# Optimization experiments

Hardware: AMD Instinct MI355X
Metric: run time of the kernel (lower is better)

## Reference

```python
import jax, jax.numpy as jnp
import numpy as np

N = 20000        # nodes
E = 160000       # directed edges (self-loops added in reference, as PyG GATConv does)
IN = 128         # in_channels
OUT = 128        # out_channels
H = 36           # heads of conv1 (head kwarg)
C = 36           # per-head channels of conv1 (== head kwarg)
HID = H * C      # 1296, conv1 concat output
NEG_SLOPE = 0.2  # PyG GATConv default


def gat_layer(x, src, dst, W, a_src, a_dst, bias, heads, ch, concat, num_nodes):
    """One PyG-style GATConv (eval mode, self-loops already in src/dst)."""
    h = (x @ W).reshape(num_nodes, heads, ch)               # [N,H,C]
    alpha_s = jnp.sum(h * a_src, axis=-1)                   # [N,H]
    alpha_d = jnp.sum(h * a_dst, axis=-1)                   # [N,H]
    e = jax.nn.leaky_relu(alpha_s[src] + alpha_d[dst], NEG_SLOPE)  # [E,H]
    # segment softmax over incoming edges of each target node
    m = jax.ops.segment_max(e, dst, num_segments=num_nodes)        # [N,H]
    m = jnp.where(jnp.isfinite(m), m, 0.0)                  # nodes with no in-edges
    ex = jnp.exp(e - m[dst])                                # [E,H]
    denom = jax.ops.segment_sum(ex, dst, num_segments=num_nodes)   # [N,H]
    alpha = ex / (denom[dst] + 1e-16)                       # [E,H]
    # weighted scatter-aggregate of source features
    out = jax.ops.segment_sum(h[src] * alpha[:, :, None], dst, num_segments=num_nodes)  # [N,H,C]
    out = out.reshape(num_nodes, heads * ch) if concat else out.mean(axis=1)
    return out + bias


def setup_inputs() -> dict:
    key = jax.random.key(0)
    ks = jax.random.split(key, 12)
    x = jax.random.normal(ks[0], (N, IN), jnp.float32)
    edge_index = jax.random.randint(ks[1], (2, E), 0, N, dtype=jnp.int64)
    # conv1 params: heads=36, out per head=36, concat
    W1 = jax.random.normal(ks[2], (IN, H * C), jnp.float32) / np.float32(np.sqrt(IN))
    a_src1 = jax.random.normal(ks[3], (H, C), jnp.float32) * 0.1
    a_dst1 = jax.random.normal(ks[4], (H, C), jnp.float32) * 0.1
    b1 = jnp.zeros((HID,), jnp.float32)
    # conv2 params: heads=1, out=OUT, no concat
    W2 = jax.random.normal(ks[5], (HID, OUT), jnp.float32) / np.float32(np.sqrt(HID))
    a_src2 = jax.random.normal(ks[6], (1, OUT), jnp.float32) * 0.1
    a_dst2 = jax.random.normal(ks[7], (1, OUT), jnp.float32) * 0.1
    b2 = jnp.zeros((OUT,), jnp.float32)
    return {"x": x, "edge_index": edge_index,
            "W1": W1, "a_src1": a_src1, "a_dst1": a_dst1, "b1": b1,
            "W2": W2, "a_src2": a_src2, "a_dst2": a_dst2, "b2": b2}


def reference(x, edge_index, W1, a_src1, a_dst1, b1, W2, a_src2, a_dst2, b2):
    num_nodes = x.shape[0]
    loop = jnp.arange(num_nodes, dtype=edge_index.dtype)
    src = jnp.concatenate([edge_index[0], loop])   # add self-loops (PyG default)
    dst = jnp.concatenate([edge_index[1], loop])
    h = jax.nn.relu(gat_layer(x, src, dst, W1, a_src1, a_dst1, b1,
                              heads=H, ch=C, concat=True, num_nodes=num_nodes))
    out = jax.nn.relu(gat_layer(h, src, dst, W2, a_src2, a_dst2, b2,
                                heads=1, ch=OUT, concat=False, num_nodes=num_nodes))
    return out
```

## Files before the change

kernel.cpp:

```cpp
#include <hip/hip_runtime.h>

#define N_NODES 20000
#define E_EDGES 160000
#define ET (E_EDGES + N_NODES)
#define IN_CH 128
#define HID 1296
#define HEADS 36
#define CPH 36
#define OUT_CH 128
#define KP2 1344
#define NEG_SLOPE 0.2f

typedef __attribute__((ext_vector_type(8))) short bf16x8;
typedef __attribute__((ext_vector_type(4))) float floatx4;

__device__ __forceinline__ float bf2f(unsigned short u) {
    union { unsigned int i; float f; } c; c.i = ((unsigned int)u) << 16; return c.f;
}
__device__ __forceinline__ unsigned short f2bf(float f) {
    union { float f; unsigned int i; } c; c.f = f;
    unsigned int r = c.i + 0x7FFF + ((c.i >> 16) & 1);
    return (unsigned short)(r >> 16);
}

#define NX (N_NODES * IN_CH / 4)
#define NW1 (HID * IN_CH)
#define NW2 (OUT_CH * KP2)
__global__ __launch_bounds__(256) void k_prep(const float* __restrict__ x,
                                              unsigned short* __restrict__ xb,
                                              const float* __restrict__ W1,
                                              unsigned short* __restrict__ W1T,
                                              const float* __restrict__ W2,
                                              unsigned short* __restrict__ W2T) {
    int gid = blockIdx.x * 256 + threadIdx.x;
    if (gid < NX) {
        float4 v = ((const float4*)x)[gid];
        ushort4 o; o.x = f2bf(v.x); o.y = f2bf(v.y); o.z = f2bf(v.z); o.w = f2bf(v.w);
        ((ushort4*)xb)[gid] = o;
    } else if (gid < NX + NW1) {
        int g = gid - NX;
        int n = g >> 7, k = g & 127;
        W1T[g] = f2bf(W1[(size_t)k * HID + n]);
    } else if (gid < NX + NW1 + NW2) {
        int g = gid - NX - NW1;
        int n = g / KP2, k = g - n * KP2;
        W2T[g] = (k < HID) ? f2bf(W2[(size_t)k * OUT_CH + n]) : 0;
    }
}

__global__ __launch_bounds__(256) void k_gemm1(const unsigned short* __restrict__ xb,
                                               const unsigned short* __restrict__ W1T,
                                               unsigned short* __restrict__ h1b) {
    __shared__ unsigned short As[128][136];
    __shared__ unsigned short Bs[64][136];
    int tid = threadIdx.x;
    int r0 = blockIdx.x * 128;
    int n0 = blockIdx.y * 64;
#pragma unroll
    for (int i = 0; i < 8; i++) {
        int c = tid + i * 256;
        int row = c >> 4, kc = (c & 15) * 8;
        int gr = min(r0 + row, N_NODES - 1);
        *(bf16x8*)&As[row][kc] = *(const bf16x8*)(xb + (size_t)gr * IN_CH + kc);
    }
#pragma unroll
    for (int i = 0; i < 4; i++) {
        int c = tid + i * 256;
        int row = c >> 4, kc = (c & 15) * 8;
        int gn = min(n0 + row, HID - 1);
        *(bf16x8*)&Bs[row][kc] = *(const bf16x8*)(W1T + (size_t)gn * IN_CH + kc);
    }
    __syncthreads();
    int lane = tid & 63, w = tid >> 6;
    int quad = lane >> 4, l15 = lane & 15;
    int mbase = w * 32;
    floatx4 acc[2][4];
#pragma unroll
    for (int i = 0; i < 2; i++)
#pragma unroll
        for (int j = 0; j < 4; j++) acc[i][j] = (floatx4){0.f, 0.f, 0.f, 0.f};
#pragma unroll
    for (int kc = 0; kc < 128; kc += 32) {
        bf16x8 a0 = *(const bf16x8*)&As[mbase + l15][kc + quad * 8];
        bf16x8 a1 = *(const bf16x8*)&As[mbase + 16 + l15][kc + quad * 8];
#pragma unroll
        for (int j = 0; j < 4; j++) {
            bf16x8 b = *(const bf16x8*)&Bs[j * 16 + l15][kc + quad * 8];
            acc[0][j] = __builtin_amdgcn_mfma_f32_16x16x32_bf16(a0, b, acc[0][j], 0, 0, 0);
            acc[1][j] = __builtin_amdgcn_mfma_f32_16x16x32_bf16(a1, b, acc[1][j], 0, 0, 0);
        }
    }
#pragma unroll
    for (int i = 0; i < 2; i++)
#pragma unroll
        for (int j = 0; j < 4; j++) {
            int colc = n0 + j * 16 + l15;
            if (colc >= HID) continue;
#pragma unroll
            for (int r = 0; r < 4; r++) {
                int row = r0 + mbase + i * 16 + quad * 4 + r;
                if (row < N_NODES)
                    h1b[(size_t)row * HID + colc] = f2bf(acc[i][j][r]);
            }
        }
}

__global__ __launch_bounds__(256) void k_gemm2(const unsigned short* __restrict__ A,
                                               const unsigned short* __restrict__ W2T,
                                               float* __restrict__ h2a,
                                               float* __restrict__ h2b) {
    __shared__ unsigned short As[32][40];
    __shared__ unsigned short Bs[128][40];
    int tid = threadIdx.x;
    int r0 = blockIdx.x * 32;
    int kbase = blockIdx.y * 672;
    int lane = tid & 63, w = tid >> 6;
    int quad = lane >> 4, l15 = lane & 15;
    int nbase = w * 32;
    floatx4 acc[2][2];
#pragma unroll
    for (int i = 0; i < 2; i++)
#pragma unroll
        for (int j = 0; j < 2; j++) acc[i][j] = (floatx4){0.f, 0.f, 0.f, 0.f};

    for (int it = 0; it < 21; it++) {
        int k0 = kbase + it * 32;
        __syncthreads();
        if (tid < 128) {
            int row = tid >> 2, kc = (tid & 3) * 8;
            *(bf16x8*)&As[row][kc] = *(const bf16x8*)(A + (size_t)(r0 + row) * KP2 + k0 + kc);
        }
#pragma unroll
        for (int i = 0; i < 2; i++) {
            int c = tid + i * 256;
            int row = c >> 2, kc = (c & 3) * 8;
            *(bf16x8*)&Bs[row][kc] = *(const bf16x8*)(W2T + (size_t)row * KP2 + k0 + kc);
        }
        __syncthreads();
        bf16x8 a0 = *(const bf16x8*)&As[l15][quad * 8];
        bf16x8 a1 = *(const bf16x8*)&As[16 + l15][quad * 8];
        bf16x8 b0 = *(const bf16x8*)&Bs[nbase + l15][quad * 8];
        bf16x8 b1 = *(const bf16x8*)&Bs[nbase + 16 + l15][quad * 8];
        acc[0][0] = __builtin_amdgcn_mfma_f32_16x16x32_bf16(a0, b0, acc[0][0], 0, 0, 0);
        acc[1][0] = __builtin_amdgcn_mfma_f32_16x16x32_bf16(a1, b0, acc[1][0], 0, 0, 0);
        acc[0][1] = __builtin_amdgcn_mfma_f32_16x16x32_bf16(a0, b1, acc[0][1], 0, 0, 0);
        acc[1][1] = __builtin_amdgcn_mfma_f32_16x16x32_bf16(a1, b1, acc[1][1], 0, 0, 0);
    }
    float* dst = (blockIdx.y == 0) ? h2a : h2b;
#pragma unroll
    for (int i = 0; i < 2; i++)
#pragma unroll
        for (int j = 0; j < 2; j++) {
            int colc = nbase + j * 16 + l15;
#pragma unroll
            for (int r = 0; r < 4; r++) {
                int row = r0 + i * 16 + quad * 4 + r;
                dst[(size_t)row * OUT_CH + colc] = acc[i][j][r];
            }
        }
}

__global__ __launch_bounds__(256) void k_alpha1(const unsigned short* __restrict__ h1b,
                                                const float* __restrict__ a_src,
                                                const float* __restrict__ a_dst,
                                                float* __restrict__ as,
                                                float* __restrict__ ad) {
    __shared__ float s_a[HEADS * CPH], s_b[HEADS * CPH];
    int tid = threadIdx.x;
    for (int i = tid; i < HEADS * CPH; i += 256) { s_a[i] = a_src[i]; s_b[i] = a_dst[i]; }
    __syncthreads();
    int gid = blockIdx.x * 256 + tid;
    if (gid >= N_NODES * HEADS) return;
    int n = gid / HEADS, h = gid - n * HEADS;
    const unsigned short* row = h1b + (size_t)n * HID + h * CPH;
    float ss = 0.f, sd = 0.f;
#pragma unroll
    for (int c = 0; c < CPH; c += 2) {
        uint u = *(const uint*)(row + c);
        float v0 = bf2f((unsigned short)(u & 0xFFFF));
        float v1 = bf2f((unsigned short)(u >> 16));
        ss += v0 * s_a[h * CPH + c] + v1 * s_a[h * CPH + c + 1];
        sd += v0 * s_b[h * CPH + c] + v1 * s_b[h * CPH + c + 1];
    }
    as[gid] = ss;
    ad[gid] = sd;
}

__global__ void k_count(const int* __restrict__ ei, int* __restrict__ cnt) {
    int e = blockIdx.x * 256 + threadIdx.x;
    if (e >= ET) return;
    int d = (e < E_EDGES) ? ei[E_EDGES + e] : (e - E_EDGES);
    atomicAdd(&cnt[d], 1);
}

__global__ __launch_bounds__(1024) void k_scan(const int* __restrict__ cnt, int* __restrict__ rowp) {
    __shared__ int sh[1024];
    const int PER = 20;
    int t = threadIdx.x;
    int base = t * PER;
    int local[PER];
    int sum = 0;
    for (int i = 0; i < PER; i++) {
        int idx = base + i;
        int v = (idx < N_NODES) ? cnt[idx] : 0;
        local[i] = sum;
        sum += v;
    }
    sh[t] = sum;
    __syncthreads();
    for (int off = 1; off < 1024; off <<= 1) {
        int v = (t >= off) ? sh[t - off] : 0;
        __syncthreads();
        sh[t] += v;
        __syncthreads();
    }
    int offset = (t == 0) ? 0 : sh[t - 1];
    for (int i = 0; i < PER; i++) {
        int idx = base + i;
        if (idx < N_NODES) rowp[idx] = offset + local[i];
    }
    if (t == 1023) rowp[N_NODES] = sh[1023];
}

__global__ void k_fill(const int* __restrict__ ei, const int* __restrict__ rowp,
                       int* __restrict__ cursor, int* __restrict__ col,
                       int* __restrict__ dstn) {
    int e = blockIdx.x * 256 + threadIdx.x;
    if (e >= ET) return;
    int s, d;
    if (e < E_EDGES) { s = ei[e]; d = ei[E_EDGES + e]; }
    else { s = e - E_EDGES; d = s; }
    int pos = rowp[d] + atomicAdd(&cursor[d], 1);
    col[pos] = s;
    dstn[pos] = d;
}

__global__ __launch_bounds__(256) void k_w1(const float* __restrict__ as1,
                                            const float* __restrict__ ad1,
                                            const int* __restrict__ col,
                                            const int* __restrict__ dstn,
                                            float* __restrict__ w,
                                            float* __restrict__ den) {
    int gid = blockIdx.x * 256 + threadIdx.x;
    if (gid >= ET * HEADS) return;
    int p = gid / HEADS, h = gid - p * HEADS;
    int s = col[p], d = dstn[p];
    float v = as1[(size_t)s * HEADS + h] + ad1[(size_t)d * HEADS + h];
    v = (v > 0.f) ? v : NEG_SLOPE * v;
    float ev = __expf(v);
    w[gid] = ev;
    atomicAdd(&den[(size_t)d * HEADS + h], ev);
}

__global__ __launch_bounds__(256) void k_agg1(const unsigned short* __restrict__ h1b,
                                              const float* __restrict__ w,
                                              const float* __restrict__ den,
                                              const int* __restrict__ rowp,
                                              const int* __restrict__ col,
                                              const float* __restrict__ b1,
                                              unsigned short* __restrict__ out1b) {
    int n = blockIdx.x;
    int tid = threadIdx.x;
    int r0 = rowp[n], r1 = rowp[n + 1];
    __shared__ float inv[HEADS];
    __shared__ float wsh[32 * HEADS];
    __shared__ int   csh[32];
    if (tid < HEADS) inv[tid] = 1.f / (den[(size_t)n * HEADS + tid] + 1e-16f);
    float4 acc0 = {0.f, 0.f, 0.f, 0.f}, acc1 = {0.f, 0.f, 0.f, 0.f};
    int s1 = tid;
    int s2 = tid + 256;
    bool s2v = (s2 < 324);
    int h1i = s1 / 9;
    int h2i = s2v ? s2 / 9 : 0;
    for (int p0 = r0; p0 < r1; p0 += 32) {
        int ne = min(32, r1 - p0);
        __syncthreads();
        for (int i = tid; i < ne * HEADS; i += 256) {
            wsh[i] = w[(size_t)p0 * HEADS + i] * inv[i % HEADS];
        }
        if (tid < ne) csh[tid] = col[p0 + tid];
        __syncthreads();
        int e = 0;
        for (; e + 2 <= ne; e += 2) {
            const ushort4* hA = (const ushort4*)(h1b + (size_t)csh[e] * HID);
            const ushort4* hB = (const ushort4*)(h1b + (size_t)csh[e + 1] * HID);
            ushort4 va1 = hA[s1];
            ushort4 vb1 = hB[s1];
            float wa = wsh[e * HEADS + h1i];
            float wb = wsh[(e + 1) * HEADS + h1i];
            acc0.x += wa * bf2f(va1.x) + wb * bf2f(vb1.x);
            acc0.y += wa * bf2f(va1.y) + wb * bf2f(vb1.y);
            acc0.z += wa * bf2f(va1.z) + wb * bf2f(vb1.z);
            acc0.w += wa * bf2f(va1.w) + wb * bf2f(vb1.w);
            if (s2v) {
                ushort4 va2 = hA[s2];
                ushort4 vb2 = hB[s2];
                float wa2 = wsh[e * HEADS + h2i];
                float wb2 = wsh[(e + 1) * HEADS + h2i];
                acc1.x += wa2 * bf2f(va2.x) + wb2 * bf2f(vb2.x);
                acc1.y += wa2 * bf2f(va2.y) + wb2 * bf2f(vb2.y);
                acc1.z += wa2 * bf2f(va2.z) + wb2 * bf2f(vb2.z);
                acc1.w += wa2 * bf2f(va2.w) + wb2 * bf2f(vb2.w);
            }
        }
        if (e < ne) {
            const ushort4* hA = (const ushort4*)(h1b + (size_t)csh[e] * HID);
            ushort4 va1 = hA[s1];
            float wa = wsh[e * HEADS + h1i];
            acc0.x += wa * bf2f(va1.x); acc0.y += wa * bf2f(va1.y);
            acc0.z += wa * bf2f(va1.z); acc0.w += wa * bf2f(va1.w);
            if (s2v) {
                ushort4 va2 = hA[s2];
                float wa2 = wsh[e * HEADS + h2i];
                acc1.x += wa2 * bf2f(va2.x); acc1.y += wa2 * bf2f(va2.y);
                acc1.z += wa2 * bf2f(va2.z); acc1.w += wa2 * bf2f(va2.w);
            }
        }
    }
    const float4* b4 = (const float4*)b1;
    ushort4* o4 = (ushort4*)(out1b + (size_t)n * KP2);
    {
        float4 bb = b4[s1];
        ushort4 o;
        o.x = f2bf(fmaxf(acc0.x + bb.x, 0.f)); o.y = f2bf(fmaxf(acc0.y + bb.y, 0.f));
        o.z = f2bf(fmaxf(acc0.z + bb.z, 0.f)); o.w = f2bf(fmaxf(acc0.w + bb.w, 0.f));
        o4[s1] = o;
    }
    if (s2v) {
        float4 bb = b4[s2];
        ushort4 o;
        o.x = f2bf(fmaxf(acc1.x + bb.x, 0.f)); o.y = f2bf(fmaxf(acc1.y + bb.y, 0.f));
        o.z = f2bf(fmaxf(acc1.z + bb.z, 0.f)); o.w = f2bf(fmaxf(acc1.w + bb.w, 0.f));
        o4[s2] = o;
    } else if (s2 < KP2 / 4) {
        o4[s2] = (ushort4){0, 0, 0, 0};
    }
}

__global__ __launch_bounds__(64) void k_alpha2c(const float* __restrict__ h2a,
                                                const float* __restrict__ h2b,
                                                unsigned short* __restrict__ h2q,
                                                const float* __restrict__ a_src,
                                                const float* __restrict__ a_dst,
                                                float* __restrict__ as,
                                                float* __restrict__ ad) {
    int n = blockIdx.x;
    int t = threadIdx.x;
    size_t base = (size_t)n * OUT_CH;
    float v0 = h2a[base + t] + h2b[base + t];
    float v1 = h2a[base + t + 64] + h2b[base + t + 64];
    h2q[base + t] = f2bf(v0);
    h2q[base + t + 64] = f2bf(v1);
    float ss = v0 * a_src[t] + v1 * a_src[t + 64];
    float sd = v0 * a_dst[t] + v1 * a_dst[t + 64];
    for (int off = 32; off > 0; off >>= 1) {
        ss += __shfl_down(ss, off);
        sd += __shfl_down(sd, off);
    }
    if (t == 0) { as[n] = ss; ad[n] = sd; }
}

__global__ __launch_bounds__(64) void k_agg2(const unsigned short* __restrict__ h2q,
                                             const float* __restrict__ as,
                                             const float* __restrict__ ad,
                                             const int* __restrict__ rowp,
                                             const int* __restrict__ col,
                                             const float* __restrict__ b2,
                                             float* __restrict__ out) {
    int n = blockIdx.x;
    int t = threadIdx.x;
    int r0 = rowp[n], r1 = rowp[n + 1];
    float adn = ad[n];
    float den = 0.f;
    for (int e = r0 + t; e < r1; e += 64) {
        float v = as[col[e]] + adn;
        v = (v > 0.f) ? v : NEG_SLOPE * v;
        den += __expf(v);
    }
#pragma unroll
    for (int off = 32; off > 0; off >>= 1) den += __shfl_xor(den, off);
    float inv = 1.f / (den + 1e-16f);
    __shared__ float wsh[32];
    __shared__ int csh[32];
    float acc0 = 0.f, acc1 = 0.f;
    for (int p0 = r0; p0 < r1; p0 += 32) {
        int ne = min(32, r1 - p0);
        __syncthreads();
        if (t < ne) {
            int s = col[p0 + t];
            csh[t] = s;
            float v = as[s] + adn;
            v = (v > 0.f) ? v : NEG_SLOPE * v;
            wsh[t] = __expf(v) * inv;
        }
        __syncthreads();
        int e = 0;
        for (; e + 2 <= ne; e += 2) {
            uint ua = *(const uint*)(h2q + (size_t)csh[e] * OUT_CH + t * 2);
            uint ub = *(const uint*)(h2q + (size_t)csh[e + 1] * OUT_CH + t * 2);
            float wa = wsh[e], wb = wsh[e + 1];
            acc0 += wa * bf2f((unsigned short)(ua & 0xFFFF)) + wb * bf2f((unsigned short)(ub & 0xFFFF));
            acc1 += wa * bf2f((unsigned short)(ua >> 16)) + wb * bf2f((unsigned short)(ub >> 16));
        }
        if (e < ne) {
            uint ua = *(const uint*)(h2q + (size_t)csh[e] * OUT_CH + t * 2);
            float wa = wsh[e];
            acc0 += wa * bf2f((unsigned short)(ua & 0xFFFF));
            acc1 += wa * bf2f((unsigned short)(ua >> 16));
        }
    }
    float o0 = acc0 + b2[t * 2];
    float o1 = acc1 + b2[t * 2 + 1];
    out[(size_t)n * OUT_CH + t * 2]     = (o0 > 0.f) ? o0 : 0.f;
    out[(size_t)n * OUT_CH + t * 2 + 1] = (o1 > 0.f) ? o1 : 0.f;
}

extern "C" void kernel_launch(void* const* d_in, const int* in_sizes, int n_in,
                              void* d_out, int out_size, void* d_ws, size_t ws_size,
                              hipStream_t stream) {
    const float* x      = (const float*)d_in[0];
    const int*   ei     = (const int*)d_in[1];
    const float* W1     = (const float*)d_in[2];
    const float* a_src1 = (const float*)d_in[3];
    const float* a_dst1 = (const float*)d_in[4];
    const float* b1     = (const float*)d_in[5];
    const float* W2     = (const float*)d_in[6];
    const float* a_src2 = (const float*)d_in[7];
    const float* a_dst2 = (const float*)d_in[8];
    const float* b2     = (const float*)d_in[9];
    float* out = (float*)d_out;

    unsigned short* h1b   = (unsigned short*)d_ws;
    unsigned short* out1b = h1b + (size_t)N_NODES * HID;
    unsigned short* xb    = out1b + (size_t)N_NODES * KP2;
    unsigned short* W1T   = xb + (size_t)N_NODES * IN_CH;
    unsigned short* W2T   = W1T + (size_t)HID * IN_CH;
    float* fbase = (float*)(W2T + NW2);
    float* as1  = fbase;
    float* ad1  = as1 + (size_t)N_NODES * HEADS;
    float* wbuf = ad1 + (size_t)N_NODES * HEADS;
    float* h2a  = wbuf;
    float* h2b  = wbuf + (size_t)N_NODES * OUT_CH;
    unsigned short* h2q = (unsigned short*)(wbuf + (size_t)2 * N_NODES * OUT_CH);
    float* as2  = wbuf + (size_t)ET * HEADS;
    float* ad2  = as2 + N_NODES;
    int* cnt    = (int*)(ad2 + N_NODES);
    int* cursor = cnt + N_NODES;
    float* den1 = (float*)(cursor + N_NODES);
    int* rowp   = (int*)(den1 + (size_t)N_NODES * HEADS);
    int* colx   = rowp + (N_NODES + 1);
    int* dstn   = colx + ET;

    hipMemsetAsync(cnt, 0, (size_t)(2 * N_NODES + N_NODES * HEADS) * sizeof(int), stream);

    k_prep<<<(NX + NW1 + NW2 + 255) / 256, 256, 0, stream>>>(x, xb, W1, W1T, W2, W2T);
    k_count<<<(ET + 255) / 256, 256, 0, stream>>>(ei, cnt);
    k_scan<<<1, 1024, 0, stream>>>(cnt, rowp);
    k_fill<<<(ET + 255) / 256, 256, 0, stream>>>(ei, rowp, cursor, colx, dstn);
    k_gemm1<<<dim3(157, 21), 256, 0, stream>>>(xb, W1T, h1b);
    k_alpha1<<<(N_NODES * HEADS + 255) / 256, 256, 0, stream>>>(h1b, a_src1, a_dst1, as1, ad1);
    k_w1<<<(ET * HEADS + 255) / 256, 256, 0, stream>>>(as1, ad1, colx, dstn, wbuf, den1);
    k_agg1<<<N_NODES, 256, 0, stream>>>(h1b, wbuf, den1, rowp, colx, b1, out1b);
    k_gemm2<<<dim3(625, 2), 256, 0, stream>>>(out1b, W2T, h2a, h2b);
    k_alpha2c<<<N_NODES, 64, 0, stream>>>(h2a, h2b, h2q, a_src2, a_dst2, as2, ad2);
    k_agg2<<<N_NODES, 64, 0, stream>>>(h2q, as2, ad2, rowp, colx, b2, out);
}
```

Before: 323.0 us.

## Fuse CSR fill with edge-weight computation and widen aggregation loads

Merges the CSR fill kernel and the per-edge-head attention weight kernel into one per-edge kernel that computes all 36 heads with float4 loads, which also drops the dstn array. The layer-1 aggregation now has each thread handle 8 contiguous bf16 channels with 16-byte loads and a 4-edge unroll, picking each channel's head weight by interpolating between at most two heads. Layer-2 aggregation is unrolled to 4 edges. The cost is fewer threads per edge in the fill and 4 serial atomics per float4 chunk, with only 162 of 256 threads active in the aggregation.

```diff
diff --git a/kernel.cpp b/kernel.cpp
--- a/kernel.cpp
+++ b/kernel.cpp
@@ -12,6 +12,7 @@
 #define NEG_SLOPE 0.2f
 
 typedef __attribute__((ext_vector_type(8))) short bf16x8;
+typedef __attribute__((ext_vector_type(8))) unsigned short ushort8;
 typedef __attribute__((ext_vector_type(4))) float floatx4;
 
 __device__ __forceinline__ float bf2f(unsigned short u) {
@@ -222,9 +223,10 @@
     if (t == 1023) rowp[N_NODES] = sh[1023];
 }
 
-__global__ void k_fill(const int* __restrict__ ei, const int* __restrict__ rowp,
-                       int* __restrict__ cursor, int* __restrict__ col,
-                       int* __restrict__ dstn) {
+__global__ void k_fillw(const int* __restrict__ ei, const int* __restrict__ rowp,
+                        int* __restrict__ cursor, int* __restrict__ col,
+                        const float* __restrict__ as1, const float* __restrict__ ad1,
+                        float* __restrict__ w, float* __restrict__ den) {
     int e = blockIdx.x * 256 + threadIdx.x;
     if (e >= ET) return;
     int s, d;
@@ -232,24 +234,26 @@
     else { s = e - E_EDGES; d = s; }
     int pos = rowp[d] + atomicAdd(&cursor[d], 1);
     col[pos] = s;
-    dstn[pos] = d;
-}
-
-__global__ __launch_bounds__(256) void k_w1(const float* __restrict__ as1,
-                                            const float* __restrict__ ad1,
-                                            const int* __restrict__ col,
-                                            const int* __restrict__ dstn,
-                                            float* __restrict__ w,
-                                            float* __restrict__ den) {
-    int gid = blockIdx.x * 256 + threadIdx.x;
-    if (gid >= ET * HEADS) return;
-    int p = gid / HEADS, h = gid - p * HEADS;
-    int s = col[p], d = dstn[p];
-    float v = as1[(size_t)s * HEADS + h] + ad1[(size_t)d * HEADS + h];
-    v = (v > 0.f) ? v : NEG_SLOPE * v;
-    float ev = __expf(v);
-    w[gid] = ev;
-    atomicAdd(&den[(size_t)d * HEADS + h], ev);
+    const float* asr = as1 + (size_t)s * HEADS;
+    const float* adr = ad1 + (size_t)d * HEADS;
+    float* wr = w + (size_t)pos * HEADS;
+    float* dn = den + (size_t)d * HEADS;
+#pragma unroll
+    for (int h = 0; h < HEADS; h += 4) {
+        float4 a = *(const float4*)(asr + h);
+        float4 b = *(const float4*)(adr + h);
+        float v0 = a.x + b.x, v1 = a.y + b.y, v2 = a.z + b.z, v3 = a.w + b.w;
+        v0 = (v0 > 0.f) ? v0 : NEG_SLOPE * v0;
+        v1 = (v1 > 0.f) ? v1 : NEG_SLOPE * v1;
+        v2 = (v2 > 0.f) ? v2 : NEG_SLOPE * v2;
+        v3 = (v3 > 0.f) ? v3 : NEG_SLOPE * v3;
+        float4 ev = {__expf(v0), __expf(v1), __expf(v2), __expf(v3)};
+        *(float4*)(wr + h) = ev;
+        atomicAdd(&dn[h + 0], ev.x);
+        atomicAdd(&dn[h + 1], ev.y);
+        atomicAdd(&dn[h + 2], ev.z);
+        atomicAdd(&dn[h + 3], ev.w);
+    }
 }
 
 __global__ __launch_bounds__(256) void k_agg1(const unsigned short* __restrict__ h1b,
@@ -266,74 +270,69 @@
     __shared__ float wsh[32 * HEADS];
     __shared__ int   csh[32];
     if (tid < HEADS) inv[tid] = 1.f / (den[(size_t)n * HEADS + tid] + 1e-16f);
-    float4 acc0 = {0.f, 0.f, 0.f, 0.f}, acc1 = {0.f, 0.f, 0.f, 0.f};
-    int s1 = tid;
-    int s2 = tid + 256;
-    bool s2v = (s2 < 324);
-    int h1i = s1 / 9;
-    int h2i = s2v ? s2 / 9 : 0;
+    const bool act = tid < 162;
+    int c0 = tid * 8;
+    int h0 = act ? c0 / 36 : 0;
+    int h7 = act ? (c0 + 7) / 36 : 0;
+    int split = (h0 + 1) * 36 - c0;
+    float sel[8];
+#pragma unroll
+    for (int j = 0; j < 8; j++) sel[j] = (j < split) ? 0.f : 1.f;
+    float acc[8];
+#pragma unroll
+    for (int j = 0; j < 8; j++) acc[j] = 0.f;
+
     for (int p0 = r0; p0 < r1; p0 += 32) {
         int ne = min(32, r1 - p0);
         __syncthreads();
-        for (int i = tid; i < ne * HEADS; i += 256) {
+        for (int i = tid; i < ne * HEADS; i += 256)
             wsh[i] = w[(size_t)p0 * HEADS + i] * inv[i % HEADS];
-        }
         if (tid < ne) csh[tid] = col[p0 + tid];
         __syncthreads();
-        int e = 0;
-        for (; e + 2 <= ne; e += 2) {
-            const ushort4* hA = (const ushort4*)(h1b + (size_t)csh[e] * HID);
-            const ushort4* hB = (const ushort4*)(h1b + (size_t)csh[e + 1] * HID);
-            ushort4 va1 = hA[s1];
-            ushort4 vb1 = hB[s1];
-            float wa = wsh[e * HEADS + h1i];
-            float wb = wsh[(e + 1) * HEADS + h1i];
-            acc0.x += wa * bf2f(va1.x) + wb * bf2f(vb1.x);
-            acc0.y += wa * bf2f(va1.y) + wb * bf2f(vb1.y);
-            acc0.z += wa * bf2f(va1.z) + wb * bf2f(vb1.z);
-            acc0.w += wa * bf2f(va1.w) + wb * bf2f(vb1.w);
-            if (s2v) {
-                ushort4 va2 = hA[s2];
-                ushort4 vb2 = hB[s2];
-                float wa2 = wsh[e * HEADS + h2i];
-                float wb2 = wsh[(e + 1) * HEADS + h2i];
-                acc1.x += wa2 * bf2f(va2.x) + wb2 * bf2f(vb2.x);
-                acc1.y += wa2 * bf2f(va2.y) + wb2 * bf2f(vb2.y);
-                acc1.z += wa2 * bf2f(va2.z) + wb2 * bf2f(vb2.z);
-                acc1.w += wa2 * bf2f(va2.w) + wb2 * bf2f(vb2.w);
+        if (act) {
+            int e = 0;
+            for (; e + 4 <= ne; e += 4) {
+                ushort8 v0 = *(const ushort8*)(h1b + (size_t)csh[e + 0] * HID + c0);
+                ushort8 v1 = *(const ushort8*)(h1b + (size_t)csh[e + 1] * HID + c0);
+                ushort8 v2 = *(const ushort8*)(h1b + (size_t)csh[e + 2] * HID + c0);
+                ushort8 v3 = *(const ushort8*)(h1b + (size_t)csh[e + 3] * HID + c0);
+#pragma unroll
+                for (int u = 0; u < 4; u++) {
+                    float wA = wsh[(e + u) * HEADS + h0];
+                    float dw = wsh[(e + u) * HEADS + h7] - wA;
+                    const ushort8& vv = (u == 0) ? v0 : (u == 1) ? v1 : (u == 2) ? v2 : v3;
+#pragma unroll
+                    for (int j = 0; j < 8; j++) {
+                        float wj = fmaf(sel[j], dw, wA);
+                        acc[j] = fmaf(wj, bf2f(vv[j]), acc[j]);
+                    }
+                }
             }
-        }
-        if (e < ne) {
-            const ushort4* hA = (const ushort4*)(h1b + (size_t)csh[e] * HID);
-            ushort4 va1 = hA[s1];
-            float wa = wsh[e * HEADS + h1i];
-            acc0.x += wa * bf2f(va1.x); acc0.y += wa * bf2f(va1.y);
-            acc0.z += wa * bf2f(va1.z); acc0.w += wa * bf2f(va1.w);
-            if (s2v) {
-                ushort4 va2 = hA[s2];
-                float wa2 = wsh[e * HEADS + h2i];
-                acc1.x += wa2 * bf2f(va2.x); acc1.y += wa2 * bf2f(va2.y);
-                acc1.z += wa2 * bf2f(va2.z); acc1.w += wa2 * bf2f(va2.w);
+            for (; e < ne; e++) {
+                ushort8 vv = *(const ushort8*)(h1b + (size_t)csh[e] * HID + c0);
+                float wA = wsh[e * HEADS + h0];
+                float dw = wsh[e * HEADS + h7] - wA;
+#pragma unroll
+                for (int j = 0; j < 8; j++) {
+                    float wj = fmaf(sel[j], dw, wA);
+                    acc[j] = fmaf(wj, bf2f(vv[j]), acc[j]);
+                }
             }
         }
     }
-    const float4* b4 = (const float4*)b1;
-    ushort4* o4 = (ushort4*)(out1b + (size_t)n * KP2);
-    {
-        float4 bb = b4[s1];
-        ushort4 o;
-        o.x = f2bf(fmaxf(acc0.x + bb.x, 0.f)); o.y = f2bf(fmaxf(acc0.y + bb.y, 0.f));
-        o.z = f2bf(fmaxf(acc0.z + bb.z, 0.f)); o.w = f2bf(fmaxf(acc0.w + bb.w, 0.f));
-        o4[s1] = o;
-    }
-    if (s2v) {
-        float4 bb = b4[s2];
-        ushort4 o;
-        o.x = f2bf(fmaxf(acc1.x + bb.x, 0.f)); o.y = f2bf(fmaxf(acc1.y + bb.y, 0.f));
-        o.z = f2bf(fmaxf(acc1.z + bb.z, 0.f)); o.w = f2bf(fmaxf(acc1.w + bb.w, 0.f));
-        o4[s2] = o;
-    } else if (s2 < KP2 / 4) {
-        o4[s2] = (ushort4){0, 0, 0, 0};
+    if (tid < KP2 / 8) {
+        ushort8 o;
+        if (act) {
+#pragma unroll
+            for (int j = 0; j < 8; j++) {
+                float vv = acc[j] + b1[c0 + j];
+                o[j] = f2bf(fmaxf(vv, 0.f));
+            }
+        } else {
+#pragma unroll
+            for (int j = 0; j < 8; j++) o[j] = 0;
+        }
+        *(ushort8*)(out1b + (size_t)n * KP2 + c0) = o;
     }
 }
 
@@ -395,14 +394,18 @@
         }
         __syncthreads();
         int e = 0;
-        for (; e + 2 <= ne; e += 2) {
-            uint ua = *(const uint*)(h2q + (size_t)csh[e] * OUT_CH + t * 2);
-            uint ub = *(const uint*)(h2q + (size_t)csh[e + 1] * OUT_CH + t * 2);
-            float wa = wsh[e], wb = wsh[e + 1];
-            acc0 += wa * bf2f((unsigned short)(ua & 0xFFFF)) + wb * bf2f((unsigned short)(ub & 0xFFFF));
-            acc1 += wa * bf2f((unsigned short)(ua >> 16)) + wb * bf2f((unsigned short)(ub >> 16));
-        }
-        if (e < ne) {
+        for (; e + 4 <= ne; e += 4) {
+            uint u0 = *(const uint*)(h2q + (size_t)csh[e + 0] * OUT_CH + t * 2);
+            uint u1 = *(const uint*)(h2q + (size_t)csh[e + 1] * OUT_CH + t * 2);
+            uint u2 = *(const uint*)(h2q + (size_t)csh[e + 2] * OUT_CH + t * 2);
+            uint u3 = *(const uint*)(h2q + (size_t)csh[e + 3] * OUT_CH + t * 2);
+            float w0 = wsh[e], w1 = wsh[e + 1], w2 = wsh[e + 2], w3 = wsh[e + 3];
+            acc0 += w0 * bf2f((unsigned short)(u0 & 0xFFFF)) + w1 * bf2f((unsigned short)(u1 & 0xFFFF))
+                  + w2 * bf2f((unsigned short)(u2 & 0xFFFF)) + w3 * bf2f((unsigned short)(u3 & 0xFFFF));
+            acc1 += w0 * bf2f((unsigned short)(u0 >> 16)) + w1 * bf2f((unsigned short)(u1 >> 16))
+                  + w2 * bf2f((unsigned short)(u2 >> 16)) + w3 * bf2f((unsigned short)(u3 >> 16));
+        }
+        for (; e < ne; e++) {
             uint ua = *(const uint*)(h2q + (size_t)csh[e] * OUT_CH + t * 2);
             float wa = wsh[e];
             acc0 += wa * bf2f((unsigned short)(ua & 0xFFFF));
@@ -449,17 +452,15 @@
     float* den1 = (float*)(cursor + N_NODES);
     int* rowp   = (int*)(den1 + (size_t)N_NODES * HEADS);
     int* colx   = rowp + (N_NODES + 1);
-    int* dstn   = colx + ET;
 
     hipMemsetAsync(cnt, 0, (size_t)(2 * N_NODES + N_NODES * HEADS) * sizeof(int), stream);
 
     k_prep<<<(NX + NW1 + NW2 + 255) / 256, 256, 0, stream>>>(x, xb, W1, W1T, W2, W2T);
     k_count<<<(ET + 255) / 256, 256, 0, stream>>>(ei, cnt);
     k_scan<<<1, 1024, 0, stream>>>(cnt, rowp);
-    k_fill<<<(ET + 255) / 256, 256, 0, stream>>>(ei, rowp, cursor, colx, dstn);
     k_gemm1<<<dim3(157, 21), 256, 0, stream>>>(xb, W1T, h1b);
     k_alpha1<<<(N_NODES * HEADS + 255) / 256, 256, 0, stream>>>(h1b, a_src1, a_dst1, as1, ad1);
-    k_w1<<<(ET * HEADS + 255) / 256, 256, 0, stream>>>(as1, ad1, colx, dstn, wbuf, den1);
+    k_fillw<<<(ET + 255) / 256, 256, 0, stream>>>(ei, rowp, cursor, colx, as1, ad1, wbuf, den1);
     k_agg1<<<N_NODES, 256, 0, stream>>>(h1b, wbuf, den1, rowp, colx, b1, out1b);
     k_gemm2<<<dim3(625, 2), 256, 0, stream>>>(out1b, W2T, h2a, h2b);
     k_alpha2c<<<N_NODES, 64, 0, stream>>>(h2a, h2b, h2q, a_src2, a_dst2, as2, ad2);
```

Result: slower. 614.2 us (+90.2%).
